# Kernel tuning notes

Hardware: AMD Instinct MI355X
Metric: run time of the kernel (lower is better)

## Reference

```python
import jax, jax.numpy as jnp
import numpy as np

EPS = 1e-08


def _cdist(x):
    # x: [B, N, D] -> [B, N, N] Euclidean distances, safe-sqrt for grad at 0
    diff = x[:, :, None, :] - x[:, None, :, :]          # [B, N, N, D]
    sq = jnp.sum(diff * diff, axis=-1)                   # [B, N, N]
    pos = sq > 0
    return jnp.where(pos, jnp.sqrt(jnp.where(pos, sq, 1.0)), 0.0)


def setup_inputs() -> dict:
    key = jax.random.key(0)
    k1, k2, k3 = jax.random.split(key, 3)
    B, N, D = 32, 1024, 3
    preds = jax.random.normal(k1, (B, N, D), dtype=jnp.float32)
    targets = jax.random.normal(k2, (B, N, D), dtype=jnp.float32)
    mask = jax.random.randint(k3, (B, N), 0, 2, dtype=jnp.int32)
    return {"preds": preds, "targets": targets, "mask": mask}


def reference(preds, targets, mask):
    m = mask.astype(preds.dtype)                         # [B, N]
    diag_att = m[:, :, None] * m[:, None, :]            # [B, N, N]
    dist_preds = _cdist(preds)                           # [B, N, N]
    dist_targets = _cdist(targets)                       # [B, N, N]
    dist = jnp.abs(dist_preds - dist_targets) / (dist_targets + EPS)  # relative=True
    loss = dist * diag_att
    return loss.sum() / diag_att.sum()
```

## Files before the change

### kernel.cpp

```cpp
#include <hip/hip_runtime.h>


constexpr int   NT   = 256;
constexpr int   SUBS = 32;
constexpr int   RBLK = 4;
constexpr int   NMAX = 1024;
constexpr float EPS  = 1e-8f;

__global__ __launch_bounds__(NT) void idl_block(
    const float* __restrict__ preds, const float* __restrict__ targets,
    const int* __restrict__ mask, float* __restrict__ partials,
    float* __restrict__ counts, int N)
{
    const int bid = blockIdx.x;
    const int b   = bid / SUBS;
    const int sub = bid % SUBS;
    const int tid = threadIdx.x;
    const int wid = tid >> 6, lane = tid & 63;

    __shared__ float px[NMAX], py[NMAX], pz[NMAX];
    __shared__ float qx[NMAX], qy[NMAX], qz[NMAX];
    __shared__ int   s_wt[NT / 64];
    __shared__ int   s_base;
    __shared__ float s_red[NT / 64];

    const float* pb = preds   + (size_t)b * N * 3;
    const float* tb = targets + (size_t)b * N * 3;
    const int*   mb = mask    + (size_t)b * N;

    if (tid == 0) s_base = 0;
    __syncthreads();

    for (int r = 0; r < N; r += NT) {
        const int  idx = r + tid;
        const bool act = (idx < N) && (mb[idx] != 0);
        float ppx = 0, ppy = 0, ppz = 0, ttx = 0, tty = 0, ttz = 0;
        if (act) {
            ppx = pb[idx * 3 + 0]; ppy = pb[idx * 3 + 1]; ppz = pb[idx * 3 + 2];
            ttx = tb[idx * 3 + 0]; tty = tb[idx * 3 + 1]; ttz = tb[idx * 3 + 2];
        }
        const unsigned long long bal = __ballot(act);
        if (lane == 0) s_wt[wid] = (int)__popcll(bal);
        __syncthreads();
        int off = s_base;
        for (int w = 0; w < wid; ++w) off += s_wt[w];
        int tot = 0;
#pragma unroll
        for (int w = 0; w < NT / 64; ++w) tot += s_wt[w];
        if (act) {
            const int pos = off + (int)__popcll(bal & ((1ull << lane) - 1ull));
            px[pos] = ppx; py[pos] = ppy; pz[pos] = ppz;
            qx[pos] = ttx; qy[pos] = tty; qz[pos] = ttz;
        }
        __syncthreads();
        if (tid == 0) s_base += tot;
        __syncthreads();
    }

    const int K   = s_base;
    const int rpc = (K + SUBS - 1) / SUBS;
    const int r0  = min(sub * rpc, K);
    const int r1  = min(r0 + rpc, K);

    float acc = 0.0f;
    for (int rg = r0; rg < r1; rg += RBLK) {
        float rpx[RBLK], rpy[RBLK], rpz[RBLK];
        float rtx[RBLK], rty[RBLK], rtz[RBLK];
        bool  rv[RBLK];
#pragma unroll
        for (int k = 0; k < RBLK; ++k) {
            const int rr = rg + k;
            rv[k] = rr < r1;
            const int i = rv[k] ? rr : r0;
            rpx[k] = px[i]; rpy[k] = py[i]; rpz[k] = pz[i];
            rtx[k] = qx[i]; rty[k] = qy[i]; rtz[k] = qz[i];
        }
        for (int j = tid; j < K; j += NT) {
            const float jpx = px[j], jpy = py[j], jpz = pz[j];
            const float jtx = qx[j], jty = qy[j], jtz = qz[j];
#pragma unroll
            for (int k = 0; k < RBLK; ++k) {
                if (rv[k]) {
                    float dx = jpx - rpx[k], dy = jpy - rpy[k], dz = jpz - rpz[k];
                    float dp = __builtin_amdgcn_sqrtf(fmaf(dx, dx, fmaf(dy, dy, dz * dz)));
                    float ex = jtx - rtx[k], ey = jty - rty[k], ez = jtz - rtz[k];
                    float dt = __builtin_amdgcn_sqrtf(fmaf(ex, ex, fmaf(ey, ey, ez * ez)));
                    acc = fmaf(fabsf(dp - dt), __builtin_amdgcn_rcpf(dt + EPS), acc);
                }
            }
        }
    }

    for (int off = 32; off > 0; off >>= 1) acc += __shfl_down(acc, off, 64);
    if ((tid & 63) == 0) s_red[tid >> 6] = acc;
    __syncthreads();
    if (tid == 0) {
        float s = 0.0f;
#pragma unroll
        for (int w = 0; w < NT / 64; ++w) s += s_red[w];
        partials[bid] = s;
        if (sub == 0) counts[b] = (float)K;
    }
}

__global__ __launch_bounds__(NT) void idl_final(
    const float* __restrict__ partials, int nP,
    const float* __restrict__ counts, int B, float* __restrict__ out)
{
    __shared__ float s_n[NT / 64], s_d[NT / 64];
    const int tid = threadIdx.x;
    float num = 0.0f, den = 0.0f;
    for (int i = tid; i < nP; i += NT) num += partials[i];
    for (int i = tid; i < B;  i += NT) { const float c = counts[i]; den = fmaf(c, c, den); }
    for (int off = 32; off > 0; off >>= 1) {
        num += __shfl_down(num, off, 64);
        den += __shfl_down(den, off, 64);
    }
    if ((tid & 63) == 0) { s_n[tid >> 6] = num; s_d[tid >> 6] = den; }
    __syncthreads();
    if (tid == 0) {
        float n = 0.0f, d = 0.0f;
#pragma unroll
        for (int w = 0; w < NT / 64; ++w) { n += s_n[w]; d += s_d[w]; }
        out[0] = n / d;
    }
}

extern "C" void kernel_launch(void* const* d_in, const int* in_sizes, int n_in,
                              void* d_out, int out_size, void* d_ws, size_t ws_size,
                              hipStream_t stream)
{
    const float* preds   = (const float*)d_in[0];
    const float* targets = (const float*)d_in[1];
    const int*   mask    = (const int*)d_in[2];
    const int N = 1024;
    const int B = in_sizes[2] / N;
    float* ws = (float*)d_ws;

    const int nBlocks = B * SUBS;
    float* partials = ws;
    float* counts   = ws + nBlocks;

    idl_block<<<dim3(nBlocks), NT, 0, stream>>>(preds, targets, mask, partials, counts, N);
    idl_final<<<dim3(1), NT, 0, stream>>>(partials, nBlocks, counts, B, (float*)d_out);
}
```

Before: 18.17 us.

## Exploit pair symmetry with upper-triangular block tiling of compacted points

```diff
diff --git a/kernel.cpp b/kernel.cpp
--- a/kernel.cpp
+++ b/kernel.cpp
@@ -1,105 +1,129 @@
 #include <hip/hip_runtime.h>
 
 
-constexpr int   NT   = 256;
-constexpr int   SUBS = 32;
-constexpr int   RBLK = 4;
-constexpr int   NMAX = 1024;
-constexpr float EPS  = 1e-8f;
+constexpr int NT   = 256;
+constexpr int C    = 8;
+constexpr int TRI  = C * (C + 1) / 2;
+constexpr int NMAX = 1024;
 
-__global__ __launch_bounds__(NT) void idl_block(
+__global__ __launch_bounds__(NT) void idl_tri(
     const float* __restrict__ preds, const float* __restrict__ targets,
     const int* __restrict__ mask, float* __restrict__ partials,
-    float* __restrict__ counts, int N)
+    float* __restrict__ counts)
 {
     const int bid = blockIdx.x;
-    const int b   = bid / SUBS;
-    const int sub = bid % SUBS;
-    const int tid = threadIdx.x;
-    const int wid = tid >> 6, lane = tid & 63;
+    const int b   = bid / TRI;
+    int ca = 0, cb;
+    {
+        int s = bid % TRI, rem = C;
+        while (s >= rem) { s -= rem; --rem; ++ca; }
+        cb = ca + s;
+    }
+    const int tid  = threadIdx.x;
+    const int wid  = tid >> 6, lane = tid & 63;
+    const int N    = 1024;
 
-    __shared__ float px[NMAX], py[NMAX], pz[NMAX];
-    __shared__ float qx[NMAX], qy[NMAX], qz[NMAX];
-    __shared__ int   s_wt[NT / 64];
-    __shared__ int   s_base;
-    __shared__ float s_red[NT / 64];
+    __shared__ __align__(16) float px[NMAX], py[NMAX], pz[NMAX];
+    __shared__ __align__(16) float qx[NMAX], qy[NMAX], qz[NMAX];
+    __shared__ int   s_wt[4][4];
+    __shared__ float s_red[4];
 
     const float* pb = preds   + (size_t)b * N * 3;
     const float* tb = targets + (size_t)b * N * 3;
     const int*   mb = mask    + (size_t)b * N;
 
-    if (tid == 0) s_base = 0;
+    int msk[4];
+#pragma unroll
+    for (int s = 0; s < 4; ++s) msk[s] = mb[s * NT + tid];
+    unsigned long long bal[4];
+#pragma unroll
+    for (int s = 0; s < 4; ++s) bal[s] = __ballot(msk[s] != 0);
+    if (lane == 0) {
+#pragma unroll
+        for (int s = 0; s < 4; ++s) s_wt[s][wid] = (int)__popcll(bal[s]);
+    }
     __syncthreads();
 
-    for (int r = 0; r < N; r += NT) {
-        const int  idx = r + tid;
-        const bool act = (idx < N) && (mb[idx] != 0);
-        float ppx = 0, ppy = 0, ppz = 0, ttx = 0, tty = 0, ttz = 0;
-        if (act) {
-            ppx = pb[idx * 3 + 0]; ppy = pb[idx * 3 + 1]; ppz = pb[idx * 3 + 2];
-            ttx = tb[idx * 3 + 0]; tty = tb[idx * 3 + 1]; ttz = tb[idx * 3 + 2];
+    int base[4], run = 0;
+#pragma unroll
+    for (int s = 0; s < 4; ++s) {
+#pragma unroll
+        for (int w = 0; w < 4; ++w) {
+            if (w == wid) base[s] = run;
+            run += s_wt[s][w];
         }
-        const unsigned long long bal = __ballot(act);
-        if (lane == 0) s_wt[wid] = (int)__popcll(bal);
-        __syncthreads();
-        int off = s_base;
-        for (int w = 0; w < wid; ++w) off += s_wt[w];
-        int tot = 0;
+    }
+    const int K = run;
+
+    const unsigned long long lt = (1ull << lane) - 1ull;
 #pragma unroll
-        for (int w = 0; w < NT / 64; ++w) tot += s_wt[w];
-        if (act) {
-            const int pos = off + (int)__popcll(bal & ((1ull << lane) - 1ull));
-            px[pos] = ppx; py[pos] = ppy; pz[pos] = ppz;
-            qx[pos] = ttx; qy[pos] = tty; qz[pos] = ttz;
+    for (int s = 0; s < 4; ++s) {
+        if (msk[s]) {
+            const int idx = s * NT + tid;
+            const int pos = base[s] + (int)__popcll(bal[s] & lt);
+            px[pos] = pb[idx * 3 + 0]; py[pos] = pb[idx * 3 + 1]; pz[pos] = pb[idx * 3 + 2];
+            qx[pos] = tb[idx * 3 + 0]; qy[pos] = tb[idx * 3 + 1]; qz[pos] = tb[idx * 3 + 2];
         }
-        __syncthreads();
-        if (tid == 0) s_base += tot;
-        __syncthreads();
     }
+    __syncthreads();
 
-    const int K   = s_base;
-    const int rpc = (K + SUBS - 1) / SUBS;
-    const int r0  = min(sub * rpc, K);
-    const int r1  = min(r0 + rpc, K);
+    const int ch  = 4 * ((K + 4 * C - 1) / (4 * C));
+    const int ra0 = min(ca * ch, K), ra1 = min(ra0 + ch, K);
+    const int cb0 = min(cb * ch, K), cb1 = min(cb0 + ch, K);
+    const int csz = cb1 - cb0;
+    const int rsz = ra1 - ra0;
+
+    const int rq = 4 * ((rsz + 15) / 16);
+    const int r0 = ra0 + wid * rq;
+    const int r1 = min(r0 + rq, ra1);
 
     float acc = 0.0f;
-    for (int rg = r0; rg < r1; rg += RBLK) {
-        float rpx[RBLK], rpy[RBLK], rpz[RBLK];
-        float rtx[RBLK], rty[RBLK], rtz[RBLK];
-        bool  rv[RBLK];
+    for (int cp = 0; cp * 64 < csz; ++cp) {
+        const int  jr = cp * 64 + lane;
+        const bool jv = jr < csz;
+        const int  j  = cb0 + (jv ? jr : 0);
+        const float jpx = px[j], jpy = py[j], jpz = pz[j];
+        const float jtx = qx[j], jty = qy[j], jtz = qz[j];
+
+        for (int rg = r0; rg < r1; rg += 4) {
+            const float4 r4x = *(const float4*)&px[rg];
+            const float4 r4y = *(const float4*)&py[rg];
+            const float4 r4z = *(const float4*)&pz[rg];
+            const float4 s4x = *(const float4*)&qx[rg];
+            const float4 s4y = *(const float4*)&qy[rg];
+            const float4 s4z = *(const float4*)&qz[rg];
+            const float rxa[4] = {r4x.x, r4x.y, r4x.z, r4x.w};
+            const float rya[4] = {r4y.x, r4y.y, r4y.z, r4y.w};
+            const float rza[4] = {r4z.x, r4z.y, r4z.z, r4z.w};
+            const float sxa[4] = {s4x.x, s4x.y, s4x.z, s4x.w};
+            const float sya[4] = {s4y.x, s4y.y, s4y.z, s4y.w};
+            const float sza[4] = {s4z.x, s4z.y, s4z.z, s4z.w};
+            const int nk = r1 - rg;
 #pragma unroll
-        for (int k = 0; k < RBLK; ++k) {
-            const int rr = rg + k;
-            rv[k] = rr < r1;
-            const int i = rv[k] ? rr : r0;
-            rpx[k] = px[i]; rpy[k] = py[i]; rpz[k] = pz[i];
-            rtx[k] = qx[i]; rty[k] = qy[i]; rtz[k] = qz[i];
-        }
-        for (int j = tid; j < K; j += NT) {
-            const float jpx = px[j], jpy = py[j], jpz = pz[j];
-            const float jtx = qx[j], jty = qy[j], jtz = qz[j];
-#pragma unroll
-            for (int k = 0; k < RBLK; ++k) {
-                if (rv[k]) {
-                    float dx = jpx - rpx[k], dy = jpy - rpy[k], dz = jpz - rpz[k];
-                    float dp = __builtin_amdgcn_sqrtf(fmaf(dx, dx, fmaf(dy, dy, dz * dz)));
-                    float ex = jtx - rtx[k], ey = jty - rty[k], ez = jtz - rtz[k];
-                    float dt = __builtin_amdgcn_sqrtf(fmaf(ex, ex, fmaf(ey, ey, ez * ez)));
-                    acc = fmaf(fabsf(dp - dt), __builtin_amdgcn_rcpf(dt + EPS), acc);
+            for (int k = 0; k < 4; ++k) {
+                if (k < nk) {
+                    const float dx = jpx - rxa[k], dy = jpy - rya[k], dz = jpz - rza[k];
+                    const float sp = fmaf(dx, dx, fmaf(dy, dy, dz * dz));
+                    const float dp = __builtin_amdgcn_sqrtf(sp);
+                    const float ex = jtx - sxa[k], ey = jty - sya[k], ez = jtz - sza[k];
+                    const float st = fmaf(ex, ex, fmaf(ey, ey, ez * ez));
+                    const float rr = __builtin_amdgcn_rsqf(st);
+                    const float dt = st * rr;
+                    const float t  = fabsf(dp - dt) * rr;
+                    acc += (jv && st > 0.0f) ? t : 0.0f;
                 }
             }
         }
     }
 
     for (int off = 32; off > 0; off >>= 1) acc += __shfl_down(acc, off, 64);
-    if ((tid & 63) == 0) s_red[tid >> 6] = acc;
+    if (lane == 0) s_red[wid] = acc;
     __syncthreads();
     if (tid == 0) {
-        float s = 0.0f;
-#pragma unroll
-        for (int w = 0; w < NT / 64; ++w) s += s_red[w];
-        partials[bid] = s;
-        if (sub == 0) counts[b] = (float)K;
+        float ssum = s_red[0] + s_red[1] + s_red[2] + s_red[3];
+        if (ca != cb) ssum *= 2.0f;
+        partials[bid] = ssum;
+        if (ca == 0 && cb == 0) counts[b] = (float)K;
     }
 }
 
@@ -135,12 +159,12 @@
     const int*   mask    = (const int*)d_in[2];
     const int N = 1024;
     const int B = in_sizes[2] / N;
-    float* ws = (float*)d_ws;
 
-    const int nBlocks = B * SUBS;
+    float* ws       = (float*)d_ws;
+    const int nBlocks = B * TRI;
     float* partials = ws;
     float* counts   = ws + nBlocks;
 
-    idl_block<<<dim3(nBlocks), NT, 0, stream>>>(preds, targets, mask, partials, counts, N);
-    idl_final<<<dim3(1), NT, 0, stream>>>(partials, nBlocks, counts, B, (float*)d_out);
+    idl_tri  <<<dim3(nBlocks), NT, 0, stream>>>(preds, targets, mask, partials, counts);
+    idl_final<<<dim3(1),       NT, 0, stream>>>(partials, nBlocks, counts, B, (float*)d_out);
 }
```

Result: faster. 16.70 us (-8.1%).
